# Kernel tuning notes

Hardware: AMD Instinct MI355X
Metric: run time of the kernel (lower is better)

The kernel has to match this reference:

```python
import jax, jax.numpy as jnp
import numpy as np

DIM = 256
HEADS = 8
HEAD_DIM = DIM // HEADS
B, N = 32, 8192


def setup_inputs() -> dict:
    key = jax.random.key(0)
    ks = jax.random.split(key, 12)
    s = 0.02
    return {
        "inputs": jax.random.normal(ks[0], (B, N, DIM), jnp.float32),
        "class_token": jax.random.normal(ks[1], (B, 1, DIM), jnp.float32),
        "mask": jax.random.randint(ks[2], (B, 1, N), 0, 2, jnp.int32),
        "W_kv": jax.random.normal(ks[3], (DIM, 2 * DIM), jnp.float32) * s,
        "b_kv": jnp.zeros((2 * DIM,), jnp.float32),
        "W_q": jax.random.normal(ks[4], (DIM, DIM), jnp.float32) * s,
        "b_q": jnp.zeros((DIM,), jnp.float32),
        "W_t1": jax.random.normal(ks[5], (HEADS, HEADS), jnp.float32) * 0.3,
        "b_t1": jnp.zeros((HEADS,), jnp.float32),
        "W_t2": jax.random.normal(ks[6], (HEADS, HEADS), jnp.float32) * 0.3,
        "b_t2": jnp.zeros((HEADS,), jnp.float32),
        "W_out": jax.random.normal(ks[7], (DIM, DIM), jnp.float32) * s,
        "b_out": jnp.zeros((DIM,), jnp.float32),
    }


def reference(inputs, class_token, mask, W_kv, b_kv, W_q, b_q, W_t1, b_t1, W_t2, b_t2, W_out, b_out):
    b, n, c = inputs.shape
    h, hd = HEADS, HEAD_DIM
    # K, V projections: (B,N,2C) -> (B,N,2,H,hd)
    kv = (inputs @ W_kv + b_kv).reshape(b, n, 2, h, hd)
    k = kv[:, :, 0]  # (B,N,H,hd)
    v = kv[:, :, 1]  # (B,N,H,hd)
    # Single query from class token: (B,1,C) -> (B,H,1,hd)
    q = (class_token @ W_q + b_q).reshape(b, h, 1, hd)
    # Scaled scores: (B,H,1,N)
    scores = jnp.einsum("bhqd,bnhd->bhqn", q, k) / jnp.sqrt(jnp.float32(hd))
    # Talking heads (pre-softmax): mix across head axis
    scores = jnp.einsum("bhqn,hg->bgqn", scores, W_t1) + b_t1[None, :, None, None]
    # Keras Softmax(mask): add large negative to masked positions
    m = mask.astype(scores.dtype)[:, None]  # (B,1,1,N)
    scores = scores + (1.0 - m) * (-1e9)
    attn = jax.nn.softmax(scores, axis=-1)
    # Talking heads (post-softmax)
    attn = jnp.einsum("bhqn,hg->bgqn", attn, W_t2) + b_t2[None, :, None, None]
    # Attend values: (B,H,1,hd) -> (B,1,C)
    out = jnp.einsum("bhqn,bnhd->bhqd", attn, v)
    out = out.transpose(0, 2, 1, 3).reshape(b, 1, c)
    return out @ W_out + b_out
```

## Files before the change

kernel.cpp:

```cpp
#include <hip/hip_runtime.h>

#define TDIM 256
#define THEADS 8
#define TB 32
#define TN 8192
#define NPAIR (TN/2)
#define BLK_PER_B 16
#define WAVES_PB 4
#define GW_PER_B (BLK_PER_B*WAVES_PB)
#define ITERS (NPAIR/GW_PER_B)
#define ACC_PER_B 2312
#define PPAD 2368

#if __has_builtin(__builtin_amdgcn_exp2f)
#define EXP2(x) __builtin_amdgcn_exp2f(x)
#else
#define EXP2(x) exp2f(x)
#endif

__device__ __forceinline__ float xr(float v, int m) { return v + __shfl_xor(v, m, 64); }

template<int CTRL>
__device__ __forceinline__ float dppadd(float v) {
  int t = __builtin_amdgcn_update_dpp(0, __float_as_int(v), CTRL, 0xF, 0xF, true);
  return v + __int_as_float(t);
}
__device__ __forceinline__ float swzadd16(float v) {
  int t = __builtin_amdgcn_ds_swizzle(__float_as_int(v), 0x401F);
  return v + __int_as_float(t);
}
__device__ __forceinline__ float red32(float v) {
  v = dppadd<0xB1>(v);
  v = dppadd<0x4E>(v);
  v = dppadd<0x141>(v);
  v = dppadd<0x128>(v);
  return swzadd16(v);
}

__global__ void tmca_prep(const float* __restrict__ ct, const float* __restrict__ Wq,
                          const float* __restrict__ bq, const float* __restrict__ Wkv,
                          const float* __restrict__ Wt1, float* __restrict__ w1) {
  int b = blockIdx.x, t = threadIdx.x;
  __shared__ float sct[TDIM], sq[TDIM], st1[64];
  sct[t] = ct[b * TDIM + t];
  if (t < 64) st1[t] = Wt1[t];
  __syncthreads();
  float a = bq[t];
  for (int c = 0; c < TDIM; ++c) a = fmaf(sct[c], Wq[c * TDIM + t], a);
  sq[t] = a;
  __syncthreads();
  float ph[THEADS];
  #pragma unroll
  for (int h = 0; h < THEADS; ++h) {
    float s = 0.f;
    #pragma unroll 8
    for (int d = 0; d < 32; ++d) s = fmaf(Wkv[t * 512 + h * 32 + d], sq[h * 32 + d], s);
    ph[h] = s;
  }
  const float sc = 0.17677669529663687f * 1.4426950408889634f;
  #pragma unroll
  for (int g = 0; g < THEADS; ++g) {
    float s = 0.f;
    #pragma unroll
    for (int h = 0; h < THEADS; ++h) s = fmaf(ph[h], st1[h * THEADS + g], s);
    w1[(b * THEADS + g) * TDIM + t] = s * sc;
  }
}

__global__ __launch_bounds__(256, 2) void tmca_main(
    const float* __restrict__ X, const int* __restrict__ mask,
    const float* __restrict__ w1, float* __restrict__ partial) {
  const int b = blockIdx.y, bk = blockIdx.x, tid = threadIdx.x;
  const int wv = tid >> 6, lane = tid & 63, half = lane >> 5, j = lane & 31;
  const int gw = bk * WAVES_PB + wv;

  const float4* w1b = (const float4*)(w1 + (size_t)b * THEADS * TDIM);
  float4 wg0[8], wg1[8];
  #pragma unroll
  for (int g = 0; g < 8; ++g) { wg0[g] = w1b[g * 64 + j]; wg1[g] = w1b[g * 64 + 32 + j]; }

  float4 Y0[8], Y1[8];
  float E[8];
  float4 S0 = make_float4(0, 0, 0, 0), S1 = make_float4(0, 0, 0, 0);
  #pragma unroll
  for (int g = 0; g < 8; ++g) {
    Y0[g] = make_float4(0, 0, 0, 0);
    Y1[g] = make_float4(0, 0, 0, 0);
    E[g] = 0.f;
  }

  const float4* Xb = (const float4*)(X + (size_t)b * TN * TDIM);
  const int* mb = mask + b * TN;
  const int n0 = 2 * gw + half;

  float4 A0 = Xb[(size_t)n0 * 64 + j], A1 = Xb[(size_t)n0 * 64 + 32 + j];
  int mA = mb[n0];
  float4 B0 = Xb[(size_t)(n0 + 128) * 64 + j], B1 = Xb[(size_t)(n0 + 128) * 64 + 32 + j];
  int mB = mb[n0 + 128];

  auto body = [&](float4 x0, float4 x1, int mk) {
    float fm = (float)mk;
    float pg[8];
    #pragma unroll
    for (int g = 0; g < 8; ++g)
      pg[g] = x0.x * wg0[g].x + x0.y * wg0[g].y + x0.z * wg0[g].z + x0.w * wg0[g].w
            + x1.x * wg1[g].x + x1.y * wg1[g].y + x1.z * wg1[g].z + x1.w * wg1[g].w;
    #pragma unroll
    for (int g = 0; g < 8; ++g) pg[g] = red32(pg[g]);
    #pragma unroll
    for (int g = 0; g < 8; ++g) {
      float e = EXP2(pg[g]) * fm;
      E[g] += e;
      Y0[g].x = fmaf(e, x0.x, Y0[g].x);
      Y0[g].y = fmaf(e, x0.y, Y0[g].y);
      Y0[g].z = fmaf(e, x0.z, Y0[g].z);
      Y0[g].w = fmaf(e, x0.w, Y0[g].w);
      Y1[g].x = fmaf(e, x1.x, Y1[g].x);
      Y1[g].y = fmaf(e, x1.y, Y1[g].y);
      Y1[g].z = fmaf(e, x1.z, Y1[g].z);
      Y1[g].w = fmaf(e, x1.w, Y1[g].w);
    }
    S0.x += x0.x; S0.y += x0.y; S0.z += x0.z; S0.w += x0.w;
    S1.x += x1.x; S1.y += x1.y; S1.z += x1.z; S1.w += x1.w;
  };

  for (int it = 0; it < ITERS - 2; it += 2) {
    {
      float4 x0 = A0, x1 = A1; int mk = mA;
      int nn = n0 + 128 * (it + 2);
      A0 = Xb[(size_t)nn * 64 + j]; A1 = Xb[(size_t)nn * 64 + 32 + j]; mA = mb[nn];
      body(x0, x1, mk);
    }
    {
      float4 x0 = B0, x1 = B1; int mk = mB;
      int nn = n0 + 128 * (it + 3);
      B0 = Xb[(size_t)nn * 64 + j]; B1 = Xb[(size_t)nn * 64 + 32 + j]; mB = mb[nn];
      body(x0, x1, mk);
    }
  }
  body(A0, A1, mA);
  body(B0, B1, mB);

  #pragma unroll
  for (int g = 0; g < 8; ++g) {
    Y0[g].x = xr(Y0[g].x, 32); Y0[g].y = xr(Y0[g].y, 32);
    Y0[g].z = xr(Y0[g].z, 32); Y0[g].w = xr(Y0[g].w, 32);
    Y1[g].x = xr(Y1[g].x, 32); Y1[g].y = xr(Y1[g].y, 32);
    Y1[g].z = xr(Y1[g].z, 32); Y1[g].w = xr(Y1[g].w, 32);
    E[g] = xr(E[g], 32);
  }
  S0.x = xr(S0.x, 32); S0.y = xr(S0.y, 32); S0.z = xr(S0.z, 32); S0.w = xr(S0.w, 32);
  S1.x = xr(S1.x, 32); S1.y = xr(S1.y, 32); S1.z = xr(S1.z, 32); S1.w = xr(S1.w, 32);

  __shared__ float red[WAVES_PB][ACC_PER_B];
  float* sl = red[wv];
  if (lane < 32) {
    #pragma unroll
    for (int g = 0; g < 8; ++g) {
      ((float4*)(sl + g * TDIM))[j] = Y0[g];
      ((float4*)(sl + g * TDIM + 128))[j] = Y1[g];
    }
    ((float4*)(sl + 2056))[j] = S0;
    ((float4*)(sl + 2056 + 128))[j] = S1;
    if (lane == 0) {
      #pragma unroll
      for (int g = 0; g < 8; ++g) sl[2048 + g] = E[g];
    }
  }
  __syncthreads();
  float* pb = partial + (size_t)(b * BLK_PER_B + bk) * PPAD;
  for (int idx = tid; idx < ACC_PER_B; idx += 256)
    pb[idx] = red[0][idx] + red[1][idx] + red[2][idx] + red[3][idx];
}

__global__ void tmca_fin(const float* __restrict__ partial, const float* __restrict__ Wkv,
                         const float* __restrict__ bkv, const float* __restrict__ Wt2,
                         const float* __restrict__ bt2, const float* __restrict__ Wout,
                         const float* __restrict__ bout, float* __restrict__ out) {
  int b = blockIdx.x, t = threadIdx.x;
  __shared__ float sacc[ACC_PER_B];
  __shared__ float z[THEADS][TDIM];
  __shared__ float opre[TDIM];
  __shared__ float sWt2[64], sbt2[8];
  const float* pb = partial + (size_t)b * BLK_PER_B * PPAD;
  for (int idx = t; idx < ACC_PER_B; idx += 256) {
    float s = 0.f;
    #pragma unroll
    for (int k = 0; k < BLK_PER_B; ++k) s += pb[(size_t)k * PPAD + idx];
    sacc[idx] = s;
  }
  if (t < 64) sWt2[t] = Wt2[t];
  if (t < 8) sbt2[t] = bt2[t];
  __syncthreads();
  float Yc[THEADS];
  #pragma unroll
  for (int g = 0; g < THEADS; ++g) Yc[g] = sacc[g * TDIM + t] / sacc[2048 + g];
  float Sc = sacc[2056 + t];
  #pragma unroll
  for (int g2 = 0; g2 < THEADS; ++g2) {
    float a = 0.f;
    #pragma unroll
    for (int g = 0; g < THEADS; ++g) a = fmaf(sWt2[g * THEADS + g2], Yc[g], a);
    z[g2][t] = a + sbt2[g2] * Sc;
  }
  __syncthreads();
  {
    int g2 = t >> 5;
    float T = 0.f;
    #pragma unroll
    for (int g = 0; g < THEADS; ++g) T += sWt2[g * THEADS + g2];
    T += (float)TN * sbt2[g2];
    float a = 0.f;
    for (int c = 0; c < TDIM; ++c) a = fmaf(z[g2][c], Wkv[c * 512 + 256 + t], a);
    opre[t] = a + T * bkv[256 + t];
  }
  __syncthreads();
  float a = bout[t];
  for (int c = 0; c < TDIM; ++c) a = fmaf(opre[c], Wout[c * TDIM + t], a);
  out[b * TDIM + t] = a;
}

extern "C" void kernel_launch(void* const* d_in, const int* in_sizes, int n_in,
                              void* d_out, int out_size, void* d_ws, size_t ws_size,
                              hipStream_t stream) {
  const float* X    = (const float*)d_in[0];
  const float* ct   = (const float*)d_in[1];
  const int*   msk  = (const int*)d_in[2];
  const float* Wkv  = (const float*)d_in[3];
  const float* bkv  = (const float*)d_in[4];
  const float* Wq   = (const float*)d_in[5];
  const float* bq   = (const float*)d_in[6];
  const float* Wt1  = (const float*)d_in[7];
  const float* Wt2  = (const float*)d_in[9];
  const float* bt2  = (const float*)d_in[10];
  const float* Wout = (const float*)d_in[11];
  const float* bout = (const float*)d_in[12];
  float* out = (float*)d_out;

  float* ws      = (float*)d_ws;
  float* w1      = ws;
  float* partial = ws + TB * THEADS * TDIM;

  hipLaunchKernelGGL(tmca_prep, dim3(TB), dim3(256), 0, stream, ct, Wq, bq, Wkv, Wt1, w1);
  hipLaunchKernelGGL(tmca_main, dim3(BLK_PER_B, TB), dim3(256), 0, stream, X, msk, w1, partial);
  hipLaunchKernelGGL(tmca_fin, dim3(TB), dim3(256), 0, stream, partial, Wkv, bkv, Wt2, bt2,
                     Wout, bout, out);
}
```

Measured before the change: 431.5 us.

## Process one row per full wave to halve registers and double occupancy

The main kernel now has each 64-lane wave handle a single token row, with one float4 per lane, instead of two rows split across half-waves. This halves the per-lane accumulator and weight registers. Occupancy goes from 2 to 4 blocks per SM, blocks per batch double to 32, and prefetching is 4-deep with wave-uniform row indices. The costs are an extra cross-half shuffle in every score reduction, twice as many partial sums for the finishing kernel to combine, and less memory-level parallelism per wave.

```diff
diff --git a/kernel.cpp b/kernel.cpp
--- a/kernel.cpp
+++ b/kernel.cpp
@@ -4,11 +4,10 @@
 #define THEADS 8
 #define TB 32
 #define TN 8192
-#define NPAIR (TN/2)
-#define BLK_PER_B 16
+#define BLK_PER_B 32
 #define WAVES_PB 4
-#define GW_PER_B (BLK_PER_B*WAVES_PB)
-#define ITERS (NPAIR/GW_PER_B)
+#define WV_PER_B (BLK_PER_B*WAVES_PB)
+#define ITERS (TN/WV_PER_B)
 #define ACC_PER_B 2312
 #define PPAD 2368
 
@@ -18,8 +17,6 @@
 #define EXP2(x) exp2f(x)
 #endif
 
-__device__ __forceinline__ float xr(float v, int m) { return v + __shfl_xor(v, m, 64); }
-
 template<int CTRL>
 __device__ __forceinline__ float dppadd(float v) {
   int t = __builtin_amdgcn_update_dpp(0, __float_as_int(v), CTRL, 0xF, 0xF, true);
@@ -29,12 +26,13 @@
   int t = __builtin_amdgcn_ds_swizzle(__float_as_int(v), 0x401F);
   return v + __int_as_float(t);
 }
-__device__ __forceinline__ float red32(float v) {
+__device__ __forceinline__ float red64(float v) {
   v = dppadd<0xB1>(v);
   v = dppadd<0x4E>(v);
   v = dppadd<0x141>(v);
   v = dppadd<0x128>(v);
-  return swzadd16(v);
+  v = swzadd16(v);
+  return v + __shfl_xor(v, 32, 64);
 }
 
 __global__ void tmca_prep(const float* __restrict__ ct, const float* __restrict__ Wq,
@@ -67,105 +65,81 @@
   }
 }
 
-__global__ __launch_bounds__(256, 2) void tmca_main(
+__global__ __launch_bounds__(256, 4) void tmca_main(
     const float* __restrict__ X, const int* __restrict__ mask,
     const float* __restrict__ w1, float* __restrict__ partial) {
   const int b = blockIdx.y, bk = blockIdx.x, tid = threadIdx.x;
-  const int wv = tid >> 6, lane = tid & 63, half = lane >> 5, j = lane & 31;
-  const int gw = bk * WAVES_PB + wv;
+  const int wv = tid >> 6, j = tid & 63;
+  const int nb = __builtin_amdgcn_readfirstlane(bk * WAVES_PB + wv);
 
   const float4* w1b = (const float4*)(w1 + (size_t)b * THEADS * TDIM);
-  float4 wg0[8], wg1[8];
-  #pragma unroll
-  for (int g = 0; g < 8; ++g) { wg0[g] = w1b[g * 64 + j]; wg1[g] = w1b[g * 64 + 32 + j]; }
-
-  float4 Y0[8], Y1[8];
+  float4 wg[8];
+  #pragma unroll
+  for (int g = 0; g < 8; ++g) wg[g] = w1b[g * 64 + j];
+
+  float4 Y[8];
   float E[8];
-  float4 S0 = make_float4(0, 0, 0, 0), S1 = make_float4(0, 0, 0, 0);
-  #pragma unroll
-  for (int g = 0; g < 8; ++g) {
-    Y0[g] = make_float4(0, 0, 0, 0);
-    Y1[g] = make_float4(0, 0, 0, 0);
-    E[g] = 0.f;
-  }
-
-  const float4* Xb = (const float4*)(X + (size_t)b * TN * TDIM);
-  const int* mb = mask + b * TN;
-  const int n0 = 2 * gw + half;
-
-  float4 A0 = Xb[(size_t)n0 * 64 + j], A1 = Xb[(size_t)n0 * 64 + 32 + j];
-  int mA = mb[n0];
-  float4 B0 = Xb[(size_t)(n0 + 128) * 64 + j], B1 = Xb[(size_t)(n0 + 128) * 64 + 32 + j];
-  int mB = mb[n0 + 128];
-
-  auto body = [&](float4 x0, float4 x1, int mk) {
-    float fm = (float)mk;
+  float4 S = make_float4(0, 0, 0, 0);
+  #pragma unroll
+  for (int g = 0; g < 8; ++g) { Y[g] = make_float4(0, 0, 0, 0); E[g] = 0.f; }
+
+  const float4* Xq = (const float4*)(X + (size_t)b * TN * TDIM) + (size_t)nb * 64 + j;
+  const int* mb = mask + b * TN + nb;
+
+  auto body = [&](float4 x, float fm) {
     float pg[8];
     #pragma unroll
     for (int g = 0; g < 8; ++g)
-      pg[g] = x0.x * wg0[g].x + x0.y * wg0[g].y + x0.z * wg0[g].z + x0.w * wg0[g].w
-            + x1.x * wg1[g].x + x1.y * wg1[g].y + x1.z * wg1[g].z + x1.w * wg1[g].w;
-    #pragma unroll
-    for (int g = 0; g < 8; ++g) pg[g] = red32(pg[g]);
+      pg[g] = x.x * wg[g].x + x.y * wg[g].y + x.z * wg[g].z + x.w * wg[g].w;
+    #pragma unroll
+    for (int g = 0; g < 8; ++g) pg[g] = red64(pg[g]);
     #pragma unroll
     for (int g = 0; g < 8; ++g) {
       float e = EXP2(pg[g]) * fm;
       E[g] += e;
-      Y0[g].x = fmaf(e, x0.x, Y0[g].x);
-      Y0[g].y = fmaf(e, x0.y, Y0[g].y);
-      Y0[g].z = fmaf(e, x0.z, Y0[g].z);
-      Y0[g].w = fmaf(e, x0.w, Y0[g].w);
-      Y1[g].x = fmaf(e, x1.x, Y1[g].x);
-      Y1[g].y = fmaf(e, x1.y, Y1[g].y);
-      Y1[g].z = fmaf(e, x1.z, Y1[g].z);
-      Y1[g].w = fmaf(e, x1.w, Y1[g].w);
-    }
-    S0.x += x0.x; S0.y += x0.y; S0.z += x0.z; S0.w += x0.w;
-    S1.x += x1.x; S1.y += x1.y; S1.z += x1.z; S1.w += x1.w;
+      Y[g].x = fmaf(e, x.x, Y[g].x);
+      Y[g].y = fmaf(e, x.y, Y[g].y);
+      Y[g].z = fmaf(e, x.z, Y[g].z);
+      Y[g].w = fmaf(e, x.w, Y[g].w);
+    }
+    S.x += x.x; S.y += x.y; S.z += x.z; S.w += x.w;
   };
 
-  for (int it = 0; it < ITERS - 2; it += 2) {
-    {
-      float4 x0 = A0, x1 = A1; int mk = mA;
-      int nn = n0 + 128 * (it + 2);
-      A0 = Xb[(size_t)nn * 64 + j]; A1 = Xb[(size_t)nn * 64 + 32 + j]; mA = mb[nn];
-      body(x0, x1, mk);
-    }
-    {
-      float4 x0 = B0, x1 = B1; int mk = mB;
-      int nn = n0 + 128 * (it + 3);
-      B0 = Xb[(size_t)nn * 64 + j]; B1 = Xb[(size_t)nn * 64 + 32 + j]; mB = mb[nn];
-      body(x0, x1, mk);
-    }
-  }
-  body(A0, A1, mA);
-  body(B0, B1, mB);
-
-  #pragma unroll
-  for (int g = 0; g < 8; ++g) {
-    Y0[g].x = xr(Y0[g].x, 32); Y0[g].y = xr(Y0[g].y, 32);
-    Y0[g].z = xr(Y0[g].z, 32); Y0[g].w = xr(Y0[g].w, 32);
-    Y1[g].x = xr(Y1[g].x, 32); Y1[g].y = xr(Y1[g].y, 32);
-    Y1[g].z = xr(Y1[g].z, 32); Y1[g].w = xr(Y1[g].w, 32);
-    E[g] = xr(E[g], 32);
-  }
-  S0.x = xr(S0.x, 32); S0.y = xr(S0.y, 32); S0.z = xr(S0.z, 32); S0.w = xr(S0.w, 32);
-  S1.x = xr(S1.x, 32); S1.y = xr(S1.y, 32); S1.z = xr(S1.z, 32); S1.w = xr(S1.w, 32);
+  float4 PA = Xq[0uL * 8192], PB = Xq[1uL * 8192], PC = Xq[2uL * 8192], PD = Xq[3uL * 8192];
+  int mA = mb[0 * 128], mB = mb[1 * 128], mC = mb[2 * 128], mD = mb[3 * 128];
+
+  for (int it = 0; it < ITERS; it += 4) {
+    const bool pf = (it + 4 < ITERS);
+    {
+      float4 x = PA; float fm = (float)mA;
+      if (pf) { PA = Xq[(size_t)(it + 4) * 8192]; mA = mb[(it + 4) * 128]; }
+      body(x, fm);
+    }
+    {
+      float4 x = PB; float fm = (float)mB;
+      if (pf) { PB = Xq[(size_t)(it + 5) * 8192]; mB = mb[(it + 5) * 128]; }
+      body(x, fm);
+    }
+    {
+      float4 x = PC; float fm = (float)mC;
+      if (pf) { PC = Xq[(size_t)(it + 6) * 8192]; mC = mb[(it + 6) * 128]; }
+      body(x, fm);
+    }
+    {
+      float4 x = PD; float fm = (float)mD;
+      if (pf) { PD = Xq[(size_t)(it + 7) * 8192]; mD = mb[(it + 7) * 128]; }
+      body(x, fm);
+    }
+  }
 
   __shared__ float red[WAVES_PB][ACC_PER_B];
   float* sl = red[wv];
-  if (lane < 32) {
-    #pragma unroll
-    for (int g = 0; g < 8; ++g) {
-      ((float4*)(sl + g * TDIM))[j] = Y0[g];
-      ((float4*)(sl + g * TDIM + 128))[j] = Y1[g];
-    }
-    ((float4*)(sl + 2056))[j] = S0;
-    ((float4*)(sl + 2056 + 128))[j] = S1;
-    if (lane == 0) {
-      #pragma unroll
-      for (int g = 0; g < 8; ++g) sl[2048 + g] = E[g];
-    }
+  #pragma unroll
+  for (int g = 0; g < 8; ++g) ((float4*)(sl + g * TDIM))[j] = Y[g];
+  ((float4*)(sl + 2056))[j] = S;
+  if (j == 0) {
+    #pragma unroll
+    for (int g = 0; g < 8; ++g) sl[2048 + g] = E[g];
   }
   __syncthreads();
   float* pb = partial + (size_t)(b * BLK_PER_B + bk) * PPAD;
@@ -185,7 +159,7 @@
   const float* pb = partial + (size_t)b * BLK_PER_B * PPAD;
   for (int idx = t; idx < ACC_PER_B; idx += 256) {
     float s = 0.f;
-    #pragma unroll
+    #pragma unroll 8
     for (int k = 0; k < BLK_PER_B; ++k) s += pb[(size_t)k * PPAD + idx];
     sacc[idx] = s;
   }
```

Result: slower. 607.2 us (+40.7%).
